# Kernel tuning notes

Hardware: AMD Instinct MI355X
Metric: run time of the kernel (lower is better)

## Reference

```python
import jax, jax.numpy as jnp
import numpy as np

N_NODES = 100000
N_EDGES = 1600000
IN_C = 128
HID_C = 128   # 2 * out_channels
OUT_C = 64


def gcn_conv(x, row, col, w, W, b, num_nodes):
    """PyG GCNConv: linear transform, add self-loops (weight 1),
    symmetric degree normalization, scatter-sum aggregation, bias."""
    h = x @ W  # [N, C_out]
    loop = jnp.arange(num_nodes, dtype=row.dtype)
    r = jnp.concatenate([row, loop])
    c = jnp.concatenate([col, loop])
    ew = jnp.concatenate([w, jnp.ones((num_nodes,), dtype=w.dtype)])
    deg = jax.ops.segment_sum(ew, c, num_segments=num_nodes)
    dinv = jnp.where(deg > 0, jax.lax.rsqrt(deg), 0.0)
    norm = dinv[r] * ew * dinv[c]            # [E+N]
    msg = h[r] * norm[:, None]               # [E+N, C_out] gather
    out = jax.ops.segment_sum(msg, c, num_segments=num_nodes)
    return out + b


def setup_inputs() -> dict:
    key = jax.random.key(0)
    k1, k2, k3, k4, k5, k6, k7, k8 = jax.random.split(key, 8)
    x = jax.random.normal(k1, (N_NODES, IN_C), dtype=jnp.float32)
    edge_index = jax.random.randint(k2, (2, N_EDGES), 0, N_NODES, dtype=jnp.int64)
    edge_weight = jax.random.uniform(k3, (N_EDGES,), dtype=jnp.float32)
    s1 = float(np.sqrt(6.0 / (IN_C + HID_C)))
    s2 = float(np.sqrt(6.0 / (HID_C + OUT_C)))
    W1 = jax.random.uniform(k4, (IN_C, HID_C), minval=-s1, maxval=s1, dtype=jnp.float32)
    b1 = jnp.zeros((HID_C,), dtype=jnp.float32)
    W2 = jax.random.uniform(k5, (HID_C, OUT_C), minval=-s2, maxval=s2, dtype=jnp.float32)
    b2 = jnp.zeros((OUT_C,), dtype=jnp.float32)
    return {"x": x, "edge_index": edge_index, "edge_weight": edge_weight,
            "W1": W1, "b1": b1, "W2": W2, "b2": b2}


def reference(x, edge_index, edge_weight, W1, b1, W2, b2):
    row, col = edge_index[0], edge_index[1]
    n = x.shape[0]
    h = jax.nn.relu(gcn_conv(x, row, col, edge_weight, W1, b1, n))
    h = jax.nn.relu(gcn_conv(h, row, col, edge_weight, W2, b2, n))
    return h
```

## Files before the change

kernel.cpp:

```cpp
#include <hip/hip_runtime.h>

#define TPB 256

typedef unsigned int uint32;
typedef unsigned short ushort_t;
typedef __attribute__((ext_vector_type(8))) short bf16x8;
typedef __attribute__((ext_vector_type(4))) float f32x4;

constexpr int NB = 256;
constexpr int B1 = 256;

__device__ __forceinline__ uint32 pack_bf16x2(float a, float b) {
  uint32 ua = __float_as_uint(a), ub = __float_as_uint(b);
  ua += 0x7FFFu + ((ua >> 16) & 1u);
  ub += 0x7FFFu + ((ub >> 16) & 1u);
  return (ua >> 16) | (ub & 0xFFFF0000u);
}
__device__ __forceinline__ ushort_t bf16_of(float a) {
  uint32 u = __float_as_uint(a);
  u += 0x7FFFu + ((u >> 16) & 1u);
  return (ushort_t)(u >> 16);
}
__device__ __forceinline__ float bf16_lo(uint32 u) { return __uint_as_float(u << 16); }
__device__ __forceinline__ float bf16_hi(uint32 u) { return __uint_as_float(u & 0xFFFF0000u); }
__device__ __forceinline__ int edge_src(uint32 e) { return (int)(e >> 15); }
__device__ __forceinline__ float edge_w(uint32 e) { return __uint_as_float((e & 0x7FFFu) << 16); }
__device__ __forceinline__ float ubf0(uint32 u) { return (float)(u & 0xFFu); }
__device__ __forceinline__ float ubf1(uint32 u) { return (float)((u >> 8) & 0xFFu); }
__device__ __forceinline__ float ubf2(uint32 u) { return (float)((u >> 16) & 0xFFu); }
__device__ __forceinline__ float ubf3(uint32 u) { return (float)((u >> 24) & 0xFFu); }

__global__ __launch_bounds__(256) void rx_hist(const int* __restrict__ col,
                                               int* __restrict__ blockhist, int e, int chunk,
                                               const float* __restrict__ W1, ushort_t* __restrict__ Wt1,
                                               const float* __restrict__ W2, ushort_t* __restrict__ Wt2,
                                               const float* __restrict__ b1, float* __restrict__ b1p) {
  __shared__ int h[NB];
  int tid = threadIdx.x, blk = blockIdx.x;
  h[tid] = 0;
  __syncthreads();
  int s = blk * chunk, t = min(e, s + chunk);
  for (int i = s + tid; i < t; i += 256) atomicAdd(&h[col[i] & 255], 1);
  int gtid = blk * 256 + tid;
  if (gtid < 128 * 128) {
    int k = gtid >> 7, m = gtid & 127;
    Wt1[m * 128 + k] = bf16_of(W1[gtid]);
  } else if (gtid < 128 * 128 + 128 * 64) {
    int j = gtid - 128 * 128;
    int k = j >> 6, m = j & 63;
    int kp = ((k & 15) << 3) | (k >> 4);
    Wt2[m * 128 + kp] = bf16_of(W2[j]);
  } else if (gtid < 128 * 128 + 128 * 64 + 128) {
    int p = gtid - (128 * 128 + 128 * 64);
    b1p[p] = b1[16 * (p & 7) + (p >> 3)];
  }
  __syncthreads();
  blockhist[tid * B1 + blk] = h[tid];
}

__global__ __launch_bounds__(256) void k_scan1(int* __restrict__ a, int* __restrict__ bsum, int n) {
  __shared__ int s[256];
  int tid = threadIdx.x;
  int base = blockIdx.x * 1024 + tid * 4;
  int v0 = 0, v1 = 0, v2 = 0, v3 = 0;
  if (base + 0 < n) v0 = a[base + 0];
  if (base + 1 < n) v1 = a[base + 1];
  if (base + 2 < n) v2 = a[base + 2];
  if (base + 3 < n) v3 = a[base + 3];
  int tsum = v0 + v1 + v2 + v3;
  s[tid] = tsum;
  __syncthreads();
  for (int off = 1; off < 256; off <<= 1) {
    int t = (tid >= off) ? s[tid - off] : 0;
    __syncthreads();
    s[tid] += t;
    __syncthreads();
  }
  if (tid == 255) bsum[blockIdx.x] = s[255];
  int e0 = s[tid] - tsum;
  int e1 = e0 + v0, e2 = e1 + v1, e3 = e2 + v2;
  if (base + 0 < n) a[base + 0] = e0;
  if (base + 1 < n) a[base + 1] = e1;
  if (base + 2 < n) a[base + 2] = e2;
  if (base + 3 < n) a[base + 3] = e3;
}

__global__ __launch_bounds__(256) void k_scan2(int* __restrict__ bsum, int nb) {
  __shared__ int s[256];
  int tid = threadIdx.x;
  int v = (tid < nb) ? bsum[tid] : 0;
  s[tid] = v;
  __syncthreads();
  for (int off = 1; off < 256; off <<= 1) {
    int t = (tid >= off) ? s[tid - off] : 0;
    __syncthreads();
    s[tid] += t;
    __syncthreads();
  }
  if (tid < nb) bsum[tid] = s[tid] - v;
}

__global__ __launch_bounds__(256) void rx_scatter1(const int* __restrict__ row,
                                                   const int* __restrict__ col,
                                                   const float* __restrict__ w,
                                                   const int* __restrict__ scanned,
                                                   const int* __restrict__ bsum,
                                                   int2* __restrict__ rec, int e, int chunk) {
  __shared__ int cur[NB];
  int tid = threadIdx.x, blk = blockIdx.x;
  int idx = tid * B1 + blk;
  cur[tid] = scanned[idx] + bsum[idx >> 10];
  __syncthreads();
  int s = blk * chunk, t = min(e, s + chunk);
  for (int i = s + tid; i < t; i += 256) {
    int c = col[i];
    int p = atomicAdd(&cur[c & 255], 1);
    rec[p] = make_int2(row[i] | ((c >> 8) << 20), __float_as_int(w[i]));
  }
}

__global__ __launch_bounds__(256) void rx_build(const int2* __restrict__ rec,
                                                const int* __restrict__ scanned,
                                                const int* __restrict__ bsum,
                                                int2* __restrict__ nodeRange,
                                                float* __restrict__ dinv,
                                                uint32* __restrict__ edges, int n, int e) {
  constexpr int NH = 512;
  __shared__ int cnt[NH];
  __shared__ int pref[NH];
  __shared__ int cur[NH];
  __shared__ float dw[NH];
  __shared__ int ssum[256];
  int tid = threadIdx.x, lo = blockIdx.x;
  int si = lo * B1;
  int s = scanned[si] + bsum[si >> 10];
  int t;
  if (lo == NB - 1) t = e;
  else {
    int ti = (lo + 1) * B1;
    t = scanned[ti] + bsum[ti >> 10];
  }
  cnt[tid] = 0; cnt[tid + 256] = 0;
  dw[tid] = 0.f; dw[tid + 256] = 0.f;
  __syncthreads();
  for (int i = s + tid; i < t; i += 256) {
    int2 r = rec[i];
    int hi = ((uint32)r.x) >> 20;
    atomicAdd(&cnt[hi], 1);
    atomicAdd(&dw[hi], __int_as_float(r.y));
  }
  __syncthreads();
  int a0 = cnt[2 * tid], a1 = cnt[2 * tid + 1];
  int sum2 = a0 + a1;
  ssum[tid] = sum2;
  __syncthreads();
  for (int off = 1; off < 256; off <<= 1) {
    int v = (tid >= off) ? ssum[tid - off] : 0;
    __syncthreads();
    ssum[tid] += v;
    __syncthreads();
  }
  int excl = ssum[tid] - sum2;
  pref[2 * tid] = excl;
  pref[2 * tid + 1] = excl + a0;
  __syncthreads();
#pragma unroll
  for (int k = 0; k < 2; ++k) {
    int hi = tid + k * 256;
    int node = (hi << 8) | lo;
    cur[hi] = s + pref[hi];
    if (node < n) {
      nodeRange[node] = make_int2(s + pref[hi], cnt[hi]);
      dinv[node] = rsqrtf(1.0f + dw[hi]);
    }
  }
  __syncthreads();
  for (int i = s + tid; i < t; i += 256) {
    int2 r = rec[i];
    int hi = ((uint32)r.x) >> 20;
    int p = atomicAdd(&cur[hi], 1);
    uint32 src = (uint32)(r.x & 0x1FFFF);
    uint32 wb = (uint32)bf16_of(__int_as_float(r.y)) & 0x7FFFu;
    edges[p] = (src << 15) | wb;
  }
}

template <int M, bool XF32, bool SWZ>
__global__ __launch_bounds__(256) void k_gemm_q(
    const void* __restrict__ Xv, const ushort_t* __restrict__ Wt,
    const float* __restrict__ dinv, unsigned char* __restrict__ Hb8,
    float* __restrict__ sc, int n) {
  __shared__ __align__(16) char smem[16384 + M * 256];
  char* Xs = smem;
  char* Ws = smem + 16384;
  const int tid = threadIdx.x;
  const int lane = tid & 63;
  const int w = tid >> 6;
  const int row0 = blockIdx.x * 64;

  {
    const uint4* src = (const uint4*)Wt;
    for (int idx = tid; idx < M * 16; idx += 256) {
      int r = idx >> 4, g = idx & 15;
      uint4 v = src[idx];
      *(uint4*)(Ws + ((r << 8) | ((g << 4) ^ ((r & 7) << 4)))) = v;
    }
  }
  if constexpr (XF32) {
    const float4* src = (const float4*)Xv;
    for (int idx = tid; idx < 64 * 16; idx += 256) {
      int r = idx >> 4, g = idx & 15;
      int grow = row0 + r;
      float4 va = make_float4(0.f, 0.f, 0.f, 0.f), vb = va;
      if (grow < n) {
        va = src[(size_t)grow * 32 + g * 2];
        vb = src[(size_t)grow * 32 + g * 2 + 1];
      }
      uint4 p;
      p.x = pack_bf16x2(va.x, va.y);
      p.y = pack_bf16x2(va.z, va.w);
      p.z = pack_bf16x2(vb.x, vb.y);
      p.w = pack_bf16x2(vb.z, vb.w);
      *(uint4*)(Xs + ((r << 8) | ((g << 4) ^ ((r & 7) << 4)))) = p;
    }
  } else {
    const uint4* src = (const uint4*)Xv;
    for (int idx = tid; idx < 64 * 16; idx += 256) {
      int r = idx >> 4, g = idx & 15;
      int grow = row0 + r;
      uint4 v = make_uint4(0u, 0u, 0u, 0u);
      if (grow < n) v = src[(size_t)grow * 16 + g];
      *(uint4*)(Xs + ((r << 8) | ((g << 4) ^ ((r & 7) << 4)))) = v;
    }
  }
  __syncthreads();

  constexpr int CT = M / 16;
  f32x4 acc[CT];
#pragma unroll
  for (int c = 0; c < CT; ++c) acc[c] = (f32x4){0.f, 0.f, 0.f, 0.f};

  const int arow = (w << 4) | (lane & 15);
  const int kb0 = (lane >> 4) << 4;
#pragma unroll
  for (int ks = 0; ks < 4; ++ks) {
    int kbyte = ks * 64 + kb0;
    bf16x8 a = *(const bf16x8*)(Xs + ((arow << 8) | (kbyte ^ ((arow & 7) << 4))));
#pragma unroll
    for (int c = 0; c < CT; ++c) {
      int brow = c * 16 + (lane & 15);
      bf16x8 b = *(const bf16x8*)(Ws + ((brow << 8) | (kbyte ^ ((brow & 7) << 4))));
      acc[c] = __builtin_amdgcn_mfma_f32_16x16x32_bf16(a, b, acc[c], 0, 0, 0);
    }
  }
  __syncthreads();

  const int gl = lane & 15;
  const int rbase = (w << 4) | ((lane >> 4) << 2);
  float mx[4] = {0.f, 0.f, 0.f, 0.f};
#pragma unroll
  for (int r = 0; r < 4; ++r) {
    int g = row0 + rbase + r;
    float dv = (g < n) ? dinv[g] : 0.f;
#pragma unroll
    for (int c = 0; c < CT; ++c) {
      acc[c][r] *= dv;
      mx[r] = fmaxf(mx[r], fabsf(acc[c][r]));
    }
  }
#pragma unroll
  for (int off = 1; off < 16; off <<= 1) {
#pragma unroll
    for (int r = 0; r < 4; ++r) mx[r] = fmaxf(mx[r], __shfl_xor(mx[r], off));
  }
  float inv[4];
#pragma unroll
  for (int r = 0; r < 4; ++r) {
    inv[r] = (mx[r] > 1e-30f) ? 127.0f / mx[r] : 0.f;
    int g = row0 + rbase + r;
    if (g < n && gl == 0) sc[g] = mx[r] * (1.0f / 127.0f);
  }

  if constexpr (SWZ) {
#pragma unroll
    for (int r = 0; r < 4; ++r) {
      int g = row0 + rbase + r;
      if (g >= n) continue;
      uint32 lo = 0, hi = 0;
#pragma unroll
      for (int c = 0; c < 4; ++c) {
        uint32 q = (uint32)((int)rintf(acc[c][r] * inv[r]) + 128);
        lo |= q << (8 * c);
      }
#pragma unroll
      for (int c = 4; c < 8; ++c) {
        uint32 q = (uint32)((int)rintf(acc[c][r] * inv[r]) + 128);
        hi |= q << (8 * (c - 4));
      }
      ((uint2*)Hb8)[(size_t)g * 16 + gl] = make_uint2(lo, hi);
    }
  } else {
    unsigned char* Cs = (unsigned char*)smem;
#pragma unroll
    for (int r = 0; r < 4; ++r) {
#pragma unroll
      for (int c = 0; c < CT; ++c) {
        int q = (int)rintf(acc[c][r] * inv[r]) + 128;
        Cs[(rbase + r) * 68 + c * 16 + gl] = (unsigned char)q;
      }
    }
    __syncthreads();
    for (int idx = tid; idx < 64 * (M / 4); idx += 256) {
      int r = idx / (M / 4), g = idx % (M / 4);
      int grow = row0 + r;
      if (grow < n)
        ((uint32*)Hb8)[(size_t)grow * (M / 4) + g] = *(const uint32*)(Cs + r * 68 + g * 4);
    }
  }
}

__global__ __launch_bounds__(TPB) void k_agg128(
    const uint2* __restrict__ t8, const float* __restrict__ scs,
    const uint32* __restrict__ edges, const int2* __restrict__ nodeRange,
    const float* __restrict__ dinv, const float* __restrict__ b1p,
    uint4* __restrict__ out, int n) {
  int node = (blockIdx.x * TPB + threadIdx.x) >> 6;
  if (node >= n) return;
  node = __builtin_amdgcn_readfirstlane(node);
  int lane = threadIdx.x & 63;
  int g = lane >> 4, gl = lane & 15;
  int2 nr = nodeRange[node];
  int s0 = nr.x, cnt = nr.y;
  int nS = min(cnt, 64);
  float di = dinv[node];
  uint32 ev = (lane < nS) ? edges[s0 + lane] : 0u;

  float a0, a1, a2, a3, a4, a5, a6, a7, beta;
  if (g == 0) {
    uint2 u = t8[(size_t)node * 16 + gl];
    float al = scs[node];
    beta = al;
    a0 = ubf0(u.x) * al; a1 = ubf1(u.x) * al; a2 = ubf2(u.x) * al; a3 = ubf3(u.x) * al;
    a4 = ubf0(u.y) * al; a5 = ubf1(u.y) * al; a6 = ubf2(u.y) * al; a7 = ubf3(u.y) * al;
  } else {
    beta = 0.f;
    a0 = a1 = a2 = a3 = a4 = a5 = a6 = a7 = 0.f;
  }
  int iters = (nS + 15) >> 4;
  int k = g;
  for (int it = 0; it < iters; ++it, k += 16) {
    uint32 e0 = __shfl(ev, k), e1 = __shfl(ev, k + 4);
    uint32 e2 = __shfl(ev, k + 8), e3 = __shfl(ev, k + 12);
    int r0 = edge_src(e0), r1 = edge_src(e1), r2 = edge_src(e2), r3 = edge_src(e3);
    uint2 v0 = t8[(size_t)r0 * 16 + gl];
    uint2 v1 = t8[(size_t)r1 * 16 + gl];
    uint2 v2 = t8[(size_t)r2 * 16 + gl];
    uint2 v3 = t8[(size_t)r3 * 16 + gl];
    float al0 = edge_w(e0) * scs[r0], al1 = edge_w(e1) * scs[r1];
    float al2 = edge_w(e2) * scs[r2], al3 = edge_w(e3) * scs[r3];
    beta += (al0 + al1) + (al2 + al3);
    a0 = fmaf(ubf0(v0.x), al0, a0); a1 = fmaf(ubf1(v0.x), al0, a1);
    a2 = fmaf(ubf2(v0.x), al0, a2); a3 = fmaf(ubf3(v0.x), al0, a3);
    a4 = fmaf(ubf0(v0.y), al0, a4); a5 = fmaf(ubf1(v0.y), al0, a5);
    a6 = fmaf(ubf2(v0.y), al0, a6); a7 = fmaf(ubf3(v0.y), al0, a7);
    a0 = fmaf(ubf0(v1.x), al1, a0); a1 = fmaf(ubf1(v1.x), al1, a1);
    a2 = fmaf(ubf2(v1.x), al1, a2); a3 = fmaf(ubf3(v1.x), al1, a3);
    a4 = fmaf(ubf0(v1.y), al1, a4); a5 = fmaf(ubf1(v1.y), al1, a5);
    a6 = fmaf(ubf2(v1.y), al1, a6); a7 = fmaf(ubf3(v1.y), al1, a7);
    a0 = fmaf(ubf0(v2.x), al2, a0); a1 = fmaf(ubf1(v2.x), al2, a1);
    a2 = fmaf(ubf2(v2.x), al2, a2); a3 = fmaf(ubf3(v2.x), al2, a3);
    a4 = fmaf(ubf0(v2.y), al2, a4); a5 = fmaf(ubf1(v2.y), al2, a5);
    a6 = fmaf(ubf2(v2.y), al2, a6); a7 = fmaf(ubf3(v2.y), al2, a7);
    a0 = fmaf(ubf0(v3.x), al3, a0); a1 = fmaf(ubf1(v3.x), al3, a1);
    a2 = fmaf(ubf2(v3.x), al3, a2); a3 = fmaf(ubf3(v3.x), al3, a3);
    a4 = fmaf(ubf0(v3.y), al3, a4); a5 = fmaf(ubf1(v3.y), al3, a5);
    a6 = fmaf(ubf2(v3.y), al3, a6); a7 = fmaf(ubf3(v3.y), al3, a7);
  }
  for (int kk = s0 + 64 + g; kk < s0 + cnt; kk += 4) {
    uint32 e0 = edges[kk];
    int r0 = edge_src(e0);
    uint2 v0 = t8[(size_t)r0 * 16 + gl];
    float al0 = edge_w(e0) * scs[r0];
    beta += al0;
    a0 = fmaf(ubf0(v0.x), al0, a0); a1 = fmaf(ubf1(v0.x), al0, a1);
    a2 = fmaf(ubf2(v0.x), al0, a2); a3 = fmaf(ubf3(v0.x), al0, a3);
    a4 = fmaf(ubf0(v0.y), al0, a4); a5 = fmaf(ubf1(v0.y), al0, a5);
    a6 = fmaf(ubf2(v0.y), al0, a6); a7 = fmaf(ubf3(v0.y), al0, a7);
  }
  a0 += __shfl_xor(a0, 16); a1 += __shfl_xor(a1, 16);
  a2 += __shfl_xor(a2, 16); a3 += __shfl_xor(a3, 16);
  a4 += __shfl_xor(a4, 16); a5 += __shfl_xor(a5, 16);
  a6 += __shfl_xor(a6, 16); a7 += __shfl_xor(a7, 16);
  beta += __shfl_xor(beta, 16);
  a0 += __shfl_xor(a0, 32); a1 += __shfl_xor(a1, 32);
  a2 += __shfl_xor(a2, 32); a3 += __shfl_xor(a3, 32);
  a4 += __shfl_xor(a4, 32); a5 += __shfl_xor(a5, 32);
  a6 += __shfl_xor(a6, 32); a7 += __shfl_xor(a7, 32);
  beta += __shfl_xor(beta, 32);
  if (g == 0) {
    float corr = 128.0f * beta;
    float4 bb0 = ((const float4*)b1p)[gl * 2];
    float4 bb1 = ((const float4*)b1p)[gl * 2 + 1];
    float o0 = fmaxf(fmaf(a0 - corr, di, bb0.x), 0.f);
    float o1 = fmaxf(fmaf(a1 - corr, di, bb0.y), 0.f);
    float o2 = fmaxf(fmaf(a2 - corr, di, bb0.z), 0.f);
    float o3 = fmaxf(fmaf(a3 - corr, di, bb0.w), 0.f);
    float o4 = fmaxf(fmaf(a4 - corr, di, bb1.x), 0.f);
    float o5 = fmaxf(fmaf(a5 - corr, di, bb1.y), 0.f);
    float o6 = fmaxf(fmaf(a6 - corr, di, bb1.z), 0.f);
    float o7 = fmaxf(fmaf(a7 - corr, di, bb1.w), 0.f);
    uint4 ob;
    ob.x = pack_bf16x2(o0, o1);
    ob.y = pack_bf16x2(o2, o3);
    ob.z = pack_bf16x2(o4, o5);
    ob.w = pack_bf16x2(o6, o7);
    out[(size_t)node * 16 + gl] = ob;
  }
}

__global__ __launch_bounds__(TPB) void k_agg64(
    const uint2* __restrict__ t8, const float* __restrict__ scs,
    const uint32* __restrict__ edges, const int2* __restrict__ nodeRange,
    const float* __restrict__ dinv, const float* __restrict__ bias,
    float4* __restrict__ out, int n) {
  int node = (blockIdx.x * TPB + threadIdx.x) >> 6;
  if (node >= n) return;
  node = __builtin_amdgcn_readfirstlane(node);
  int lane = threadIdx.x & 63;
  int g = lane >> 3, gl = lane & 7;
  int2 nr = nodeRange[node];
  int s0 = nr.x, cnt = nr.y;
  int nS = min(cnt, 64);
  float di = dinv[node];
  uint32 ev = (lane < nS) ? edges[s0 + lane] : 0u;

  float a0, a1, a2, a3, a4, a5, a6, a7, beta;
  if (g == 0) {
    uint2 u = t8[(size_t)node * 8 + gl];
    float al = scs[node];
    beta = al;
    a0 = ubf0(u.x) * al; a1 = ubf1(u.x) * al; a2 = ubf2(u.x) * al; a3 = ubf3(u.x) * al;
    a4 = ubf0(u.y) * al; a5 = ubf1(u.y) * al; a6 = ubf2(u.y) * al; a7 = ubf3(u.y) * al;
  } else {
    beta = 0.f;
    a0 = a1 = a2 = a3 = a4 = a5 = a6 = a7 = 0.f;
  }
  int iters = (nS + 15) >> 4;
  int k = g;
  for (int it = 0; it < iters; ++it, k += 16) {
    uint32 e0 = __shfl(ev, k), e1 = __shfl(ev, k + 8);
    int r0 = edge_src(e0), r1 = edge_src(e1);
    uint2 v0 = t8[(size_t)r0 * 8 + gl];
    uint2 v1 = t8[(size_t)r1 * 8 + gl];
    float al0 = edge_w(e0) * scs[r0], al1 = edge_w(e1) * scs[r1];
    beta += al0 + al1;
    a0 = fmaf(ubf0(v0.x), al0, a0); a1 = fmaf(ubf1(v0.x), al0, a1);
    a2 = fmaf(ubf2(v0.x), al0, a2); a3 = fmaf(ubf3(v0.x), al0, a3);
    a4 = fmaf(ubf0(v0.y), al0, a4); a5 = fmaf(ubf1(v0.y), al0, a5);
    a6 = fmaf(ubf2(v0.y), al0, a6); a7 = fmaf(ubf3(v0.y), al0, a7);
    a0 = fmaf(ubf0(v1.x), al1, a0); a1 = fmaf(ubf1(v1.x), al1, a1);
    a2 = fmaf(ubf2(v1.x), al1, a2); a3 = fmaf(ubf3(v1.x), al1, a3);
    a4 = fmaf(ubf0(v1.y), al1, a4); a5 = fmaf(ubf1(v1.y), al1, a5);
    a6 = fmaf(ubf2(v1.y), al1, a6); a7 = fmaf(ubf3(v1.y), al1, a7);
  }
  for (int kk = s0 + 64 + g; kk < s0 + cnt; kk += 8) {
    uint32 e0 = edges[kk];
    int r0 = edge_src(e0);
    uint2 v0 = t8[(size_t)r0 * 8 + gl];
    float al0 = edge_w(e0) * scs[r0];
    beta += al0;
    a0 = fmaf(ubf0(v0.x), al0, a0); a1 = fmaf(ubf1(v0.x), al0, a1);
    a2 = fmaf(ubf2(v0.x), al0, a2); a3 = fmaf(ubf3(v0.x), al0, a3);
    a4 = fmaf(ubf0(v0.y), al0, a4); a5 = fmaf(ubf1(v0.y), al0, a5);
    a6 = fmaf(ubf2(v0.y), al0, a6); a7 = fmaf(ubf3(v0.y), al0, a7);
  }
#pragma unroll
  for (int off = 8; off <= 32; off <<= 1) {
    a0 += __shfl_xor(a0, off); a1 += __shfl_xor(a1, off);
    a2 += __shfl_xor(a2, off); a3 += __shfl_xor(a3, off);
    a4 += __shfl_xor(a4, off); a5 += __shfl_xor(a5, off);
    a6 += __shfl_xor(a6, off); a7 += __shfl_xor(a7, off);
    beta += __shfl_xor(beta, off);
  }
  if (g == 0) {
    float corr = 128.0f * beta;
    float4 bb0 = ((const float4*)bias)[gl * 2];
    float4 bb1 = ((const float4*)bias)[gl * 2 + 1];
    float4 o0, o1;
    o0.x = fmaxf(fmaf(a0 - corr, di, bb0.x), 0.f);
    o0.y = fmaxf(fmaf(a1 - corr, di, bb0.y), 0.f);
    o0.z = fmaxf(fmaf(a2 - corr, di, bb0.z), 0.f);
    o0.w = fmaxf(fmaf(a3 - corr, di, bb0.w), 0.f);
    o1.x = fmaxf(fmaf(a4 - corr, di, bb1.x), 0.f);
    o1.y = fmaxf(fmaf(a5 - corr, di, bb1.y), 0.f);
    o1.z = fmaxf(fmaf(a6 - corr, di, bb1.z), 0.f);
    o1.w = fmaxf(fmaf(a7 - corr, di, bb1.w), 0.f);
    out[(size_t)node * 16 + gl * 2] = o0;
    out[(size_t)node * 16 + gl * 2 + 1] = o1;
  }
}

extern "C" void kernel_launch(void* const* d_in, const int* in_sizes, int n_in,
                              void* d_out, int out_size, void* d_ws, size_t ws_size,
                              hipStream_t stream) {
  const float* x  = (const float*)d_in[0];
  const int*   ei = (const int*)d_in[1];
  const float* ew = (const float*)d_in[2];
  const float* W1 = (const float*)d_in[3];
  const float* b1 = (const float*)d_in[4];
  const float* W2 = (const float*)d_in[5];
  const float* b2 = (const float*)d_in[6];
  float* out = (float*)d_out;

  constexpr int IN_C = 128, HID = 128, OUTC = 64;
  const int n = in_sizes[0] / IN_C;
  const int e = in_sizes[2];
  const int* rowp = ei;
  const int* colp = ei + e;

  auto cdiv = [](long a, long b) { return (int)((a + b - 1) / b); };
  auto align = [](size_t v) { return (v + 255) & ~(size_t)255; };

  char* ws = (char*)d_ws;
  size_t o = 0;
  int*      blockhist = (int*)(ws + o);      o = align(o + (size_t)NB * B1 * 4);
  int*      bsum      = (int*)(ws + o);      o = align(o + 4096);
  float*    dinv      = (float*)(ws + o);    o = align(o + (size_t)n * 4);
  int2*     nodeRange = (int2*)(ws + o);     o = align(o + (size_t)n * 8);
  ushort_t* Wt1       = (ushort_t*)(ws + o); o = align(o + (size_t)HID * IN_C * 2);
  ushort_t* Wt2       = (ushort_t*)(ws + o); o = align(o + (size_t)OUTC * HID * 2);
  float*    b1p       = (float*)(ws + o);    o = align(o + 512);
  float*    sc1       = (float*)(ws + o);    o = align(o + (size_t)n * 4);
  float*    sc2       = (float*)(ws + o);    o = align(o + (size_t)n * 4);
  int2*     rec       = (int2*)(ws + o);     o = align(o + (size_t)e * 8);
  uint32*   edges     = (uint32*)(ws + o);   o = align(o + (size_t)e * 4);
  unsigned char* hs1b8 = (unsigned char*)(ws + o); o = align(o + (size_t)n * HID);
  uint4*    o1b       = (uint4*)(ws + o);    o = align(o + (size_t)n * HID * 2);
  unsigned char* hs2b8 = hs1b8;

  const int chunk = cdiv(e, B1);
  const int nscan = NB * B1;

  rx_hist<<<B1, 256, 0, stream>>>(colp, blockhist, e, chunk, W1, Wt1, W2, Wt2, b1, b1p);
  k_scan1<<<nscan / 1024, 256, 0, stream>>>(blockhist, bsum, nscan);
  k_scan2<<<1, 256, 0, stream>>>(bsum, nscan / 1024);
  rx_scatter1<<<B1, 256, 0, stream>>>(rowp, colp, ew, blockhist, bsum, rec, e, chunk);
  rx_build<<<NB, 256, 0, stream>>>(rec, blockhist, bsum, nodeRange, dinv, edges, n, e);

  k_gemm_q<HID, true, true><<<cdiv(n, 64), 256, 0, stream>>>(x, Wt1, dinv, hs1b8, sc1, n);
  k_agg128<<<cdiv(n, 4), TPB, 0, stream>>>((const uint2*)hs1b8, sc1, edges, nodeRange,
                                           dinv, b1p, o1b, n);

  k_gemm_q<OUTC, false, false><<<cdiv(n, 64), 256, 0, stream>>>(o1b, Wt2, dinv, hs2b8, sc2, n);
  k_agg64<<<cdiv(n, 4), TPB, 0, stream>>>((const uint2*)hs2b8, sc2, edges, nodeRange,
                                          dinv, b2, (float4*)out, n);
}
```

Before: 175.9 us.

## Aggregate with int8 sdot4 using per-node quantized edge coefficients

Switches the stored features from unsigned-offset to signed int8 and quantizes each node's edge coefficients (alpha) to int8 per wavefront, so the aggregation uses sdot4 integer dot products on byte-permuted feature vectors instead of per-element float FMAs. The self-loop is folded into the edge list as lane 0, removing the separate self term and the beta offset correction. Both aggregation kernels are merged into one template, and groups whose packed coefficients are all zero skip their gathers. This cuts ALU work in the gather loop but adds extra quantization error from the int8 coefficients, plus shuffle and permute overhead.

```diff
diff --git a/kernel.cpp b/kernel.cpp
--- a/kernel.cpp
+++ b/kernel.cpp
@@ -21,14 +21,24 @@
   u += 0x7FFFu + ((u >> 16) & 1u);
   return (ushort_t)(u >> 16);
 }
-__device__ __forceinline__ float bf16_lo(uint32 u) { return __uint_as_float(u << 16); }
-__device__ __forceinline__ float bf16_hi(uint32 u) { return __uint_as_float(u & 0xFFFF0000u); }
-__device__ __forceinline__ int edge_src(uint32 e) { return (int)(e >> 15); }
 __device__ __forceinline__ float edge_w(uint32 e) { return __uint_as_float((e & 0x7FFFu) << 16); }
-__device__ __forceinline__ float ubf0(uint32 u) { return (float)(u & 0xFFu); }
-__device__ __forceinline__ float ubf1(uint32 u) { return (float)((u >> 8) & 0xFFu); }
-__device__ __forceinline__ float ubf2(uint32 u) { return (float)((u >> 16) & 0xFFu); }
-__device__ __forceinline__ float ubf3(uint32 u) { return (float)((u >> 24) & 0xFFu); }
+__device__ __forceinline__ float sb0(uint32 u) { return (float)(int)(signed char)(u & 0xFFu); }
+__device__ __forceinline__ float sb1(uint32 u) { return (float)(int)(signed char)((u >> 8) & 0xFFu); }
+__device__ __forceinline__ float sb2(uint32 u) { return (float)(int)(signed char)((u >> 16) & 0xFFu); }
+__device__ __forceinline__ float sb3(uint32 u) { return (float)(int)(signed char)((u >> 24) & 0xFFu); }
+
+__device__ __forceinline__ int SDOT4(uint32 a, uint32 b, int c) {
+#if __has_builtin(__builtin_amdgcn_sdot4)
+  return __builtin_amdgcn_sdot4((int)a, (int)b, c, false);
+#else
+  c += (int)(signed char)(a & 0xFF) * (int)(signed char)(b & 0xFF);
+  c += (int)(signed char)((a >> 8) & 0xFF) * (int)(signed char)((b >> 8) & 0xFF);
+  c += (int)(signed char)((a >> 16) & 0xFF) * (int)(signed char)((b >> 16) & 0xFF);
+  c += (int)(signed char)((a >> 24) & 0xFF) * (int)(signed char)((b >> 24) & 0xFF);
+  return c;
+#endif
+}
+#define PERM(hi, lo, sel) __builtin_amdgcn_perm((hi), (lo), (sel))
 
 __global__ __launch_bounds__(256) void rx_hist(const int* __restrict__ col,
                                                int* __restrict__ blockhist, int e, int chunk,
@@ -289,13 +299,13 @@
       uint32 lo = 0, hi = 0;
 #pragma unroll
       for (int c = 0; c < 4; ++c) {
-        uint32 q = (uint32)((int)rintf(acc[c][r] * inv[r]) + 128);
-        lo |= q << (8 * c);
+        int q = (int)rintf(acc[c][r] * inv[r]);
+        lo |= ((uint32)(q & 0xFF)) << (8 * c);
       }
 #pragma unroll
       for (int c = 4; c < 8; ++c) {
-        uint32 q = (uint32)((int)rintf(acc[c][r] * inv[r]) + 128);
-        hi |= q << (8 * (c - 4));
+        int q = (int)rintf(acc[c][r] * inv[r]);
+        hi |= ((uint32)(q & 0xFF)) << (8 * (c - 4));
       }
       ((uint2*)Hb8)[(size_t)g * 16 + gl] = make_uint2(lo, hi);
     }
@@ -305,8 +315,8 @@
     for (int r = 0; r < 4; ++r) {
 #pragma unroll
       for (int c = 0; c < CT; ++c) {
-        int q = (int)rintf(acc[c][r] * inv[r]) + 128;
-        Cs[(rbase + r) * 68 + c * 16 + gl] = (unsigned char)q;
+        int q = (int)rintf(acc[c][r] * inv[r]);
+        Cs[(rbase + r) * 68 + c * 16 + gl] = (unsigned char)(q & 0xFF);
       }
     }
     __syncthreads();
@@ -319,184 +329,123 @@
   }
 }
 
-__global__ __launch_bounds__(TPB) void k_agg128(
+template <int GROUPS, int RS, bool BF16OUT>
+__global__ __launch_bounds__(TPB) void k_aggq(
     const uint2* __restrict__ t8, const float* __restrict__ scs,
     const uint32* __restrict__ edges, const int2* __restrict__ nodeRange,
-    const float* __restrict__ dinv, const float* __restrict__ b1p,
-    uint4* __restrict__ out, int n) {
+    const float* __restrict__ dinv, const float* __restrict__ bias,
+    void* __restrict__ out, int n) {
+  constexpr int GL = 64 / GROUPS;
   int node = (blockIdx.x * TPB + threadIdx.x) >> 6;
   if (node >= n) return;
   node = __builtin_amdgcn_readfirstlane(node);
   int lane = threadIdx.x & 63;
-  int g = lane >> 4, gl = lane & 15;
+  int g = lane / GL;
+  int gl = lane % GL;
   int2 nr = nodeRange[node];
   int s0 = nr.x, cnt = nr.y;
-  int nS = min(cnt, 64);
+  int nS = min(cnt + 1, 64);
   float di = dinv[node];
-  uint32 ev = (lane < nS) ? edges[s0 + lane] : 0u;
-
-  float a0, a1, a2, a3, a4, a5, a6, a7, beta;
+
+  uint32 ev = 0u;
+  if (lane == 0) ev = ((uint32)node << 15) | 0x3F80u;
+  else if (lane < nS) ev = edges[s0 + lane - 1];
+
+  int src = (int)(ev >> 15);
+  float alpha = edge_w(ev) * scs[src];
+  float am = alpha;
+#pragma unroll
+  for (int off = 1; off < 64; off <<= 1) am = fmaxf(am, __shfl_xor(am, off));
+  float qinv = (am > 1e-30f) ? 127.0f / am : 0.f;
+  float ascale = am * (1.0f / 127.0f);
+  int aq = (int)rintf(alpha * qinv);
+  int tt = __shfl_xor(aq, 1);
+  int bb = (lane & 1) ? (tt | (aq << 8)) : (aq | (tt << 8));
+  int t2 = __shfl_xor(bb, 2);
+  uint32 qd = (lane & 2) ? ((uint32)t2 | ((uint32)bb << 16)) : ((uint32)bb | ((uint32)t2 << 16));
+
+  int ac0 = 0, ac1 = 0, ac2 = 0, ac3 = 0, ac4 = 0, ac5 = 0, ac6 = 0, ac7 = 0;
+  int iters = (nS + 4 * GROUPS - 1) / (4 * GROUPS);
+  for (int it = 0; it < iters; ++it) {
+    int k = it * 4 * GROUPS + 4 * g;
+    uint32 Aq = __shfl(qd, k);
+    uint32 e0 = __shfl(ev, k), e1 = __shfl(ev, k + 1);
+    uint32 e2 = __shfl(ev, k + 2), e3 = __shfl(ev, k + 3);
+    if (Aq != 0u) {
+      uint2 v0 = t8[(size_t)(e0 >> 15) * RS + gl];
+      uint2 v1 = t8[(size_t)(e1 >> 15) * RS + gl];
+      uint2 v2 = t8[(size_t)(e2 >> 15) * RS + gl];
+      uint2 v3 = t8[(size_t)(e3 >> 15) * RS + gl];
+      uint32 p01a = PERM(v1.x, v0.x, 0x05010400u), p01b = PERM(v1.x, v0.x, 0x07030602u);
+      uint32 p23a = PERM(v3.x, v2.x, 0x05010400u), p23b = PERM(v3.x, v2.x, 0x07030602u);
+      uint32 d0 = PERM(p23a, p01a, 0x05040100u), d1 = PERM(p23a, p01a, 0x07060302u);
+      uint32 d2 = PERM(p23b, p01b, 0x05040100u), d3 = PERM(p23b, p01b, 0x07060302u);
+      ac0 = SDOT4(d0, Aq, ac0); ac1 = SDOT4(d1, Aq, ac1);
+      ac2 = SDOT4(d2, Aq, ac2); ac3 = SDOT4(d3, Aq, ac3);
+      p01a = PERM(v1.y, v0.y, 0x05010400u); p01b = PERM(v1.y, v0.y, 0x07030602u);
+      p23a = PERM(v3.y, v2.y, 0x05010400u); p23b = PERM(v3.y, v2.y, 0x07030602u);
+      d0 = PERM(p23a, p01a, 0x05040100u); d1 = PERM(p23a, p01a, 0x07060302u);
+      d2 = PERM(p23b, p01b, 0x05040100u); d3 = PERM(p23b, p01b, 0x07060302u);
+      ac4 = SDOT4(d0, Aq, ac4); ac5 = SDOT4(d1, Aq, ac5);
+      ac6 = SDOT4(d2, Aq, ac6); ac7 = SDOT4(d3, Aq, ac7);
+    }
+  }
+
+  float f0 = 0.f, f1 = 0.f, f2 = 0.f, f3 = 0.f, f4 = 0.f, f5 = 0.f, f6 = 0.f, f7 = 0.f;
+  bool hasTail = (cnt > 63);
+  if (hasTail) {
+    for (int kk = s0 + 63 + g; kk < s0 + cnt; kk += GROUPS) {
+      uint32 e0 = edges[kk];
+      int r0 = (int)(e0 >> 15);
+      uint2 v0 = t8[(size_t)r0 * RS + gl];
+      float al = edge_w(e0) * scs[r0];
+      f0 = fmaf(sb0(v0.x), al, f0); f1 = fmaf(sb1(v0.x), al, f1);
+      f2 = fmaf(sb2(v0.x), al, f2); f3 = fmaf(sb3(v0.x), al, f3);
+      f4 = fmaf(sb0(v0.y), al, f4); f5 = fmaf(sb1(v0.y), al, f5);
+      f6 = fmaf(sb2(v0.y), al, f6); f7 = fmaf(sb3(v0.y), al, f7);
+    }
+#pragma unroll
+    for (int off = GL; off < 64; off <<= 1) {
+      f0 += __shfl_xor(f0, off); f1 += __shfl_xor(f1, off);
+      f2 += __shfl_xor(f2, off); f3 += __shfl_xor(f3, off);
+      f4 += __shfl_xor(f4, off); f5 += __shfl_xor(f5, off);
+      f6 += __shfl_xor(f6, off); f7 += __shfl_xor(f7, off);
+    }
+  }
+
+#pragma unroll
+  for (int off = GL; off < 64; off <<= 1) {
+    ac0 += __shfl_xor(ac0, off); ac1 += __shfl_xor(ac1, off);
+    ac2 += __shfl_xor(ac2, off); ac3 += __shfl_xor(ac3, off);
+    ac4 += __shfl_xor(ac4, off); ac5 += __shfl_xor(ac5, off);
+    ac6 += __shfl_xor(ac6, off); ac7 += __shfl_xor(ac7, off);
+  }
+
   if (g == 0) {
-    uint2 u = t8[(size_t)node * 16 + gl];
-    float al = scs[node];
-    beta = al;
-    a0 = ubf0(u.x) * al; a1 = ubf1(u.x) * al; a2 = ubf2(u.x) * al; a3 = ubf3(u.x) * al;
-    a4 = ubf0(u.y) * al; a5 = ubf1(u.y) * al; a6 = ubf2(u.y) * al; a7 = ubf3(u.y) * al;
-  } else {
-    beta = 0.f;
-    a0 = a1 = a2 = a3 = a4 = a5 = a6 = a7 = 0.f;
-  }
-  int iters = (nS + 15) >> 4;
-  int k = g;
-  for (int it = 0; it < iters; ++it, k += 16) {
-    uint32 e0 = __shfl(ev, k), e1 = __shfl(ev, k + 4);
-    uint32 e2 = __shfl(ev, k + 8), e3 = __shfl(ev, k + 12);
-    int r0 = edge_src(e0), r1 = edge_src(e1), r2 = edge_src(e2), r3 = edge_src(e3);
-    uint2 v0 = t8[(size_t)r0 * 16 + gl];
-    uint2 v1 = t8[(size_t)r1 * 16 + gl];
-    uint2 v2 = t8[(size_t)r2 * 16 + gl];
-    uint2 v3 = t8[(size_t)r3 * 16 + gl];
-    float al0 = edge_w(e0) * scs[r0], al1 = edge_w(e1) * scs[r1];
-    float al2 = edge_w(e2) * scs[r2], al3 = edge_w(e3) * scs[r3];
-    beta += (al0 + al1) + (al2 + al3);
-    a0 = fmaf(ubf0(v0.x), al0, a0); a1 = fmaf(ubf1(v0.x), al0, a1);
-    a2 = fmaf(ubf2(v0.x), al0, a2); a3 = fmaf(ubf3(v0.x), al0, a3);
-    a4 = fmaf(ubf0(v0.y), al0, a4); a5 = fmaf(ubf1(v0.y), al0, a5);
-    a6 = fmaf(ubf2(v0.y), al0, a6); a7 = fmaf(ubf3(v0.y), al0, a7);
-    a0 = fmaf(ubf0(v1.x), al1, a0); a1 = fmaf(ubf1(v1.x), al1, a1);
-    a2 = fmaf(ubf2(v1.x), al1, a2); a3 = fmaf(ubf3(v1.x), al1, a3);
-    a4 = fmaf(ubf0(v1.y), al1, a4); a5 = fmaf(ubf1(v1.y), al1, a5);
-    a6 = fmaf(ubf2(v1.y), al1, a6); a7 = fmaf(ubf3(v1.y), al1, a7);
-    a0 = fmaf(ubf0(v2.x), al2, a0); a1 = fmaf(ubf1(v2.x), al2, a1);
-    a2 = fmaf(ubf2(v2.x), al2, a2); a3 = fmaf(ubf3(v2.x), al2, a3);
-    a4 = fmaf(ubf0(v2.y), al2, a4); a5 = fmaf(ubf1(v2.y), al2, a5);
-    a6 = fmaf(ubf2(v2.y), al2, a6); a7 = fmaf(ubf3(v2.y), al2, a7);
-    a0 = fmaf(ubf0(v3.x), al3, a0); a1 = fmaf(ubf1(v3.x), al3, a1);
-    a2 = fmaf(ubf2(v3.x), al3, a2); a3 = fmaf(ubf3(v3.x), al3, a3);
-    a4 = fmaf(ubf0(v3.y), al3, a4); a5 = fmaf(ubf1(v3.y), al3, a5);
-    a6 = fmaf(ubf2(v3.y), al3, a6); a7 = fmaf(ubf3(v3.y), al3, a7);
-  }
-  for (int kk = s0 + 64 + g; kk < s0 + cnt; kk += 4) {
-    uint32 e0 = edges[kk];
-    int r0 = edge_src(e0);
-    uint2 v0 = t8[(size_t)r0 * 16 + gl];
-    float al0 = edge_w(e0) * scs[r0];
-    beta += al0;
-    a0 = fmaf(ubf0(v0.x), al0, a0); a1 = fmaf(ubf1(v0.x), al0, a1);
-    a2 = fmaf(ubf2(v0.x), al0, a2); a3 = fmaf(ubf3(v0.x), al0, a3);
-    a4 = fmaf(ubf0(v0.y), al0, a4); a5 = fmaf(ubf1(v0.y), al0, a5);
-    a6 = fmaf(ubf2(v0.y), al0, a6); a7 = fmaf(ubf3(v0.y), al0, a7);
-  }
-  a0 += __shfl_xor(a0, 16); a1 += __shfl_xor(a1, 16);
-  a2 += __shfl_xor(a2, 16); a3 += __shfl_xor(a3, 16);
-  a4 += __shfl_xor(a4, 16); a5 += __shfl_xor(a5, 16);
-  a6 += __shfl_xor(a6, 16); a7 += __shfl_xor(a7, 16);
-  beta += __shfl_xor(beta, 16);
-  a0 += __shfl_xor(a0, 32); a1 += __shfl_xor(a1, 32);
-  a2 += __shfl_xor(a2, 32); a3 += __shfl_xor(a3, 32);
-  a4 += __shfl_xor(a4, 32); a5 += __shfl_xor(a5, 32);
-  a6 += __shfl_xor(a6, 32); a7 += __shfl_xor(a7, 32);
-  beta += __shfl_xor(beta, 32);
-  if (g == 0) {
-    float corr = 128.0f * beta;
-    float4 bb0 = ((const float4*)b1p)[gl * 2];
-    float4 bb1 = ((const float4*)b1p)[gl * 2 + 1];
-    float o0 = fmaxf(fmaf(a0 - corr, di, bb0.x), 0.f);
-    float o1 = fmaxf(fmaf(a1 - corr, di, bb0.y), 0.f);
-    float o2 = fmaxf(fmaf(a2 - corr, di, bb0.z), 0.f);
-    float o3 = fmaxf(fmaf(a3 - corr, di, bb0.w), 0.f);
-    float o4 = fmaxf(fmaf(a4 - corr, di, bb1.x), 0.f);
-    float o5 = fmaxf(fmaf(a5 - corr, di, bb1.y), 0.f);
-    float o6 = fmaxf(fmaf(a6 - corr, di, bb1.z), 0.f);
-    float o7 = fmaxf(fmaf(a7 - corr, di, bb1.w), 0.f);
-    uint4 ob;
-    ob.x = pack_bf16x2(o0, o1);
-    ob.y = pack_bf16x2(o2, o3);
-    ob.z = pack_bf16x2(o4, o5);
-    ob.w = pack_bf16x2(o6, o7);
-    out[(size_t)node * 16 + gl] = ob;
-  }
-}
-
-__global__ __launch_bounds__(TPB) void k_agg64(
-    const uint2* __restrict__ t8, const float* __restrict__ scs,
-    const uint32* __restrict__ edges, const int2* __restrict__ nodeRange,
-    const float* __restrict__ dinv, const float* __restrict__ bias,
-    float4* __restrict__ out, int n) {
-  int node = (blockIdx.x * TPB + threadIdx.x) >> 6;
-  if (node >= n) return;
-  node = __builtin_amdgcn_readfirstlane(node);
-  int lane = threadIdx.x & 63;
-  int g = lane >> 3, gl = lane & 7;
-  int2 nr = nodeRange[node];
-  int s0 = nr.x, cnt = nr.y;
-  int nS = min(cnt, 64);
-  float di = dinv[node];
-  uint32 ev = (lane < nS) ? edges[s0 + lane] : 0u;
-
-  float a0, a1, a2, a3, a4, a5, a6, a7, beta;
-  if (g == 0) {
-    uint2 u = t8[(size_t)node * 8 + gl];
-    float al = scs[node];
-    beta = al;
-    a0 = ubf0(u.x) * al; a1 = ubf1(u.x) * al; a2 = ubf2(u.x) * al; a3 = ubf3(u.x) * al;
-    a4 = ubf0(u.y) * al; a5 = ubf1(u.y) * al; a6 = ubf2(u.y) * al; a7 = ubf3(u.y) * al;
-  } else {
-    beta = 0.f;
-    a0 = a1 = a2 = a3 = a4 = a5 = a6 = a7 = 0.f;
-  }
-  int iters = (nS + 15) >> 4;
-  int k = g;
-  for (int it = 0; it < iters; ++it, k += 16) {
-    uint32 e0 = __shfl(ev, k), e1 = __shfl(ev, k + 8);
-    int r0 = edge_src(e0), r1 = edge_src(e1);
-    uint2 v0 = t8[(size_t)r0 * 8 + gl];
-    uint2 v1 = t8[(size_t)r1 * 8 + gl];
-    float al0 = edge_w(e0) * scs[r0], al1 = edge_w(e1) * scs[r1];
-    beta += al0 + al1;
-    a0 = fmaf(ubf0(v0.x), al0, a0); a1 = fmaf(ubf1(v0.x), al0, a1);
-    a2 = fmaf(ubf2(v0.x), al0, a2); a3 = fmaf(ubf3(v0.x), al0, a3);
-    a4 = fmaf(ubf0(v0.y), al0, a4); a5 = fmaf(ubf1(v0.y), al0, a5);
-    a6 = fmaf(ubf2(v0.y), al0, a6); a7 = fmaf(ubf3(v0.y), al0, a7);
-    a0 = fmaf(ubf0(v1.x), al1, a0); a1 = fmaf(ubf1(v1.x), al1, a1);
-    a2 = fmaf(ubf2(v1.x), al1, a2); a3 = fmaf(ubf3(v1.x), al1, a3);
-    a4 = fmaf(ubf0(v1.y), al1, a4); a5 = fmaf(ubf1(v1.y), al1, a5);
-    a6 = fmaf(ubf2(v1.y), al1, a6); a7 = fmaf(ubf3(v1.y), al1, a7);
-  }
-  for (int kk = s0 + 64 + g; kk < s0 + cnt; kk += 8) {
-    uint32 e0 = edges[kk];
-    int r0 = edge_src(e0);
-    uint2 v0 = t8[(size_t)r0 * 8 + gl];
-    float al0 = edge_w(e0) * scs[r0];
-    beta += al0;
-    a0 = fmaf(ubf0(v0.x), al0, a0); a1 = fmaf(ubf1(v0.x), al0, a1);
-    a2 = fmaf(ubf2(v0.x), al0, a2); a3 = fmaf(ubf3(v0.x), al0, a3);
-    a4 = fmaf(ubf0(v0.y), al0, a4); a5 = fmaf(ubf1(v0.y), al0, a5);
-    a6 = fmaf(ubf2(v0.y), al0, a6); a7 = fmaf(ubf3(v0.y), al0, a7);
-  }
-#pragma unroll
-  for (int off = 8; off <= 32; off <<= 1) {
-    a0 += __shfl_xor(a0, off); a1 += __shfl_xor(a1, off);
-    a2 += __shfl_xor(a2, off); a3 += __shfl_xor(a3, off);
-    a4 += __shfl_xor(a4, off); a5 += __shfl_xor(a5, off);
-    a6 += __shfl_xor(a6, off); a7 += __shfl_xor(a7, off);
-    beta += __shfl_xor(beta, off);
-  }
-  if (g == 0) {
-    float corr = 128.0f * beta;
+    float s = ascale * di;
     float4 bb0 = ((const float4*)bias)[gl * 2];
     float4 bb1 = ((const float4*)bias)[gl * 2 + 1];
-    float4 o0, o1;
-    o0.x = fmaxf(fmaf(a0 - corr, di, bb0.x), 0.f);
-    o0.y = fmaxf(fmaf(a1 - corr, di, bb0.y), 0.f);
-    o0.z = fmaxf(fmaf(a2 - corr, di, bb0.z), 0.f);
-    o0.w = fmaxf(fmaf(a3 - corr, di, bb0.w), 0.f);
-    o1.x = fmaxf(fmaf(a4 - corr, di, bb1.x), 0.f);
-    o1.y = fmaxf(fmaf(a5 - corr, di, bb1.y), 0.f);
-    o1.z = fmaxf(fmaf(a6 - corr, di, bb1.z), 0.f);
-    o1.w = fmaxf(fmaf(a7 - corr, di, bb1.w), 0.f);
-    out[(size_t)node * 16 + gl * 2] = o0;
-    out[(size_t)node * 16 + gl * 2 + 1] = o1;
+    float o0 = fmaxf(fmaf((float)ac0, s, fmaf(f0, di, bb0.x)), 0.f);
+    float o1 = fmaxf(fmaf((float)ac1, s, fmaf(f1, di, bb0.y)), 0.f);
+    float o2 = fmaxf(fmaf((float)ac2, s, fmaf(f2, di, bb0.z)), 0.f);
+    float o3 = fmaxf(fmaf((float)ac3, s, fmaf(f3, di, bb0.w)), 0.f);
+    float o4 = fmaxf(fmaf((float)ac4, s, fmaf(f4, di, bb1.x)), 0.f);
+    float o5 = fmaxf(fmaf((float)ac5, s, fmaf(f5, di, bb1.y)), 0.f);
+    float o6 = fmaxf(fmaf((float)ac6, s, fmaf(f6, di, bb1.z)), 0.f);
+    float o7 = fmaxf(fmaf((float)ac7, s, fmaf(f7, di, bb1.w)), 0.f);
+    if constexpr (BF16OUT) {
+      uint4 ob;
+      ob.x = pack_bf16x2(o0, o1);
+      ob.y = pack_bf16x2(o2, o3);
+      ob.z = pack_bf16x2(o4, o5);
+      ob.w = pack_bf16x2(o6, o7);
+      ((uint4*)out)[(size_t)node * 16 + gl] = ob;
+    } else {
+      float4 w0 = make_float4(o0, o1, o2, o3);
+      float4 w1 = make_float4(o4, o5, o6, o7);
+      ((float4*)out)[(size_t)node * 16 + gl * 2] = w0;
+      ((float4*)out)[(size_t)node * 16 + gl * 2 + 1] = w1;
+    }
   }
 }
 
@@ -548,10 +497,10 @@
   rx_build<<<NB, 256, 0, stream>>>(rec, blockhist, bsum, nodeRange, dinv, edges, n, e);
 
   k_gemm_q<HID, true, true><<<cdiv(n, 64), 256, 0, stream>>>(x, Wt1, dinv, hs1b8, sc1, n);
-  k_agg128<<<cdiv(n, 4), TPB, 0, stream>>>((const uint2*)hs1b8, sc1, edges, nodeRange,
-                                           dinv, b1p, o1b, n);
+  k_aggq<4, 16, true><<<cdiv(n, 4), TPB, 0, stream>>>((const uint2*)hs1b8, sc1, edges,
+                                                      nodeRange, dinv, b1p, o1b, n);
 
   k_gemm_q<OUTC, false, false><<<cdiv(n, 64), 256, 0, stream>>>(o1b, Wt2, dinv, hs2b8, sc2, n);
-  k_agg64<<<cdiv(n, 4), TPB, 0, stream>>>((const uint2*)hs2b8, sc2, edges, nodeRange,
-                                          dinv, b2, (float4*)out, n);
-}
+  k_aggq<8, 8, false><<<cdiv(n, 4), TPB, 0, stream>>>((const uint2*)hs2b8, sc2, edges,
+                                                      nodeRange, dinv, b2, out, n);
+}
```

After: 185.8 us. +5.7%, slower.
